# Optimization experiments

Hardware: AMD Instinct MI355X
Metric: run time of the kernel (lower is better)

## Reference

```python
import jax, jax.numpy as jnp
import numpy as np

B, S, H = 4, 1024, 1024
NH, HD = 16, 64  # num heads, head dim


def setup_inputs() -> dict:
    key = jax.random.key(0)
    ks = jax.random.split(key, 7)
    scale = 1.0 / np.sqrt(H)
    return {
        "hidden_states": jax.random.normal(ks[0], (B, S, H), jnp.float32),
        "attention_mask": jnp.zeros((B, 1, 1, S), jnp.float32),
        "Wq": jax.random.normal(ks[1], (H, H), jnp.float32) * scale,
        "bq": jnp.zeros((H,), jnp.float32),
        "Wk": jax.random.normal(ks[2], (H, H), jnp.float32) * scale,
        "bk": jnp.zeros((H,), jnp.float32),
        "Wv": jax.random.normal(ks[3], (H, H), jnp.float32) * scale,
        "bv": jnp.zeros((H,), jnp.float32),
    }


def _heads(x):
    # [B,S,H] -> [B,NH,S,HD]
    return x.reshape(x.shape[0], x.shape[1], NH, HD).transpose(0, 2, 1, 3)


def reference(hidden_states, attention_mask, Wq, bq, Wk, bk, Wv, bv):
    q = _heads(hidden_states @ Wq + bq)  # [B,NH,S,HD]
    k = _heads(hidden_states @ Wk + bk)
    v = _heads(hidden_states @ Wv + bv)
    scores = jnp.einsum("bhqd,bhkd->bhqk", q, k) / np.sqrt(HD)
    scores = scores + attention_mask  # broadcast additive mask
    probs = jax.nn.softmax(scores, axis=-1)  # dropout p=0 (eval)
    ctx = jnp.einsum("bhqk,bhkd->bhqd", probs, v)
    # [B,NH,S,HD] -> [B,S,H]
    return ctx.transpose(0, 2, 1, 3).reshape(hidden_states.shape[0], hidden_states.shape[1], NH * HD)
```

## Files before the change

### kernel.cpp

```cpp
#include <hip/hip_runtime.h>
#include <hip/hip_bf16.h>

typedef __bf16 bf16_t;
typedef __bf16 bf16x8 __attribute__((ext_vector_type(8)));
typedef float f32x4 __attribute__((ext_vector_type(4)));
typedef float f32x16 __attribute__((ext_vector_type(16)));
typedef unsigned uint2v __attribute__((ext_vector_type(2)));

#define MFMA16(a, b, c) __builtin_amdgcn_mfma_f32_16x16x32_bf16((a), (b), (c), 0, 0, 0)
#define MFMA32(a, b, c) __builtin_amdgcn_mfma_f32_32x32x16_bf16((a), (b), (c), 0, 0, 0)

static constexpr int BB = 4, SS = 1024, HH = 1024, NHEAD = 16, HDIM = 64;
static constexpr int MM = BB * SS;

__device__ __forceinline__ void gload_lds16(const void* g, void* l) {
  __builtin_amdgcn_global_load_lds((const __attribute__((address_space(1))) void*)g,
                                   (__attribute__((address_space(3))) void*)l, 16, 0, 0);
}

#if __has_builtin(__builtin_amdgcn_permlane32_swap)
#define PSWAP(a, b)                                                    \
  {                                                                    \
    uint2v _r = __builtin_amdgcn_permlane32_swap((a), (b), false, false); \
    (a) = _r.x;                                                        \
    (b) = _r.y;                                                        \
  }
#else
#define PSWAP(a, b) asm("v_permlane32_swap_b32 %0, %1" : "+v"(a), "+v"(b))
#endif

__global__ __launch_bounds__(256) void cvt_bf16_kernel(const float* __restrict__ in,
                                                       bf16_t* __restrict__ out, int n) {
  int i = (blockIdx.x * 256 + threadIdx.x) * 8;
  if (i >= n) return;
  float4 a = *(const float4*)(in + i);
  float4 b = *(const float4*)(in + i + 4);
  union { int4 i4; bf16_t h[8]; } u;
  u.h[0] = (bf16_t)a.x; u.h[1] = (bf16_t)a.y; u.h[2] = (bf16_t)a.z; u.h[3] = (bf16_t)a.w;
  u.h[4] = (bf16_t)b.x; u.h[5] = (bf16_t)b.y; u.h[6] = (bf16_t)b.z; u.h[7] = (bf16_t)b.w;
  *(int4*)(out + i) = u.i4;
}

__global__ __launch_bounds__(256) void transposeW_kernel(const float* __restrict__ Wq,
                                                         const float* __restrict__ Wk,
                                                         const float* __restrict__ Wv,
                                                         bf16_t* __restrict__ WT) {
  __shared__ float tile[32][33];
  int z = blockIdx.z;
  const float* W = (z == 0) ? Wq : (z == 1) ? Wk : Wv;
  bf16_t* Out = WT + (size_t)z * HH * HH;
  int tx = threadIdx.x, ty = threadIdx.y;
  int x0 = blockIdx.x * 32;
  int y0 = blockIdx.y * 32;
  for (int j = ty; j < 32; j += 8)
    tile[j][tx] = W[(size_t)(y0 + j) * HH + x0 + tx];
  __syncthreads();
  for (int j = ty; j < 32; j += 8)
    Out[(size_t)(x0 + j) * HH + y0 + tx] = (bf16_t)tile[tx][j];
}

#define BMT 128
#define BNT 384
#define BKT 64
#define NTL 16
#define BUFBYTES 65536

__global__ __launch_bounds__(512, 2) void qkv_gemm2(const bf16_t* __restrict__ hiddenB,
                                                    const bf16_t* __restrict__ WT,
                                                    const float* __restrict__ bq,
                                                    const float* __restrict__ bk,
                                                    const float* __restrict__ bv,
                                                    bf16_t* __restrict__ Qo,
                                                    bf16_t* __restrict__ Ko,
                                                    bf16_t* __restrict__ Vt) {
  __shared__ bf16_t smem[2 * BUFBYTES / 2];

  const int wg = blockIdx.x;
  const int id = (wg & 7) * 32 + (wg >> 3);
  const int nb = id & 7;
  const int mb = id >> 3;

  const int t = threadIdx.x;
  const int lane = t & 63;
  const int w = t >> 6;
  const int wr = w >> 2;
  const int wc = w & 3;
  const int lr = lane & 15;
  const int g4 = lane >> 4;

  const unsigned schunk = (((unsigned)(t & 7)) ^ ((unsigned)((t >> 3) & 7))) << 4;
  const char* Ag = (const char*)hiddenB + (size_t)(mb * BMT) * 2048;
  const char* Bg = (const char*)WT + (size_t)(nb * BNT) * 2048;

  auto stage = [&](const char* gb, int growbase, int kbyte, char* ldsdest) {
    gload_lds16(gb + (size_t)(growbase + (t >> 3)) * 2048 + kbyte + schunk,
                ldsdest + w * 1024);
  };
  const unsigned axor = ((unsigned)(lr & 7)) << 4;

  f32x4 acc[4][6] = {};

  {
    char* S0 = (char*)smem;
    stage(Ag, 0, 0, S0);
    stage(Ag, 64, 0, S0 + 8192);
#pragma unroll
    for (int i = 0; i < 6; ++i) stage(Bg, i * 64, 0, S0 + 16384 + i * 8192);
  }
  asm volatile("s_waitcnt vmcnt(0)" ::: "memory");
  __builtin_amdgcn_s_barrier();

  for (int j = 0; j < NTL; ++j) {
    const char* Ab = (const char*)smem + (j & 1) * BUFBYTES;
    const char* Bb = Ab + 16384;
    char* Sb = (char*)smem + ((j + 1) & 1) * BUFBYTES;
    const int kb = (j + 1) * 128;
    const bool st = (j + 1 < NTL);

    if (st) { stage(Ag, 0, kb, Sb); stage(Ag, 64, kb, Sb + 8192); }

    bf16x8 af[4][2];
#pragma unroll
    for (int mi = 0; mi < 4; ++mi)
#pragma unroll
      for (int ks = 0; ks < 2; ++ks)
        af[mi][ks] = *(const bf16x8*)(Ab + (size_t)(wr * 64 + mi * 16 + lr) * 128 +
                                      (((unsigned)(ks * 64 + g4 * 16)) ^ axor));

#pragma unroll
    for (int p = 0; p < 3; ++p) {
      if (st) {
        stage(Bg, (2 * p) * 64, kb, Sb + 16384 + (2 * p) * 8192);
        stage(Bg, (2 * p + 1) * 64, kb, Sb + 16384 + (2 * p + 1) * 8192);
      }
      bf16x8 b0[2], b1[2];
#pragma unroll
      for (int ks = 0; ks < 2; ++ks) {
        b0[ks] = *(const bf16x8*)(Bb + (size_t)(wc * 96 + (2 * p) * 16 + lr) * 128 +
                                  (((unsigned)(ks * 64 + g4 * 16)) ^ axor));
        b1[ks] = *(const bf16x8*)(Bb + (size_t)(wc * 96 + (2 * p + 1) * 16 + lr) * 128 +
                                  (((unsigned)(ks * 64 + g4 * 16)) ^ axor));
      }
      __builtin_amdgcn_s_setprio(1);
#pragma unroll
      for (int mi = 0; mi < 4; ++mi)
#pragma unroll
        for (int ks = 0; ks < 2; ++ks) {
          acc[mi][2 * p] = MFMA16(af[mi][ks], b0[ks], acc[mi][2 * p]);
          acc[mi][2 * p + 1] = MFMA16(af[mi][ks], b1[ks], acc[mi][2 * p + 1]);
        }
      __builtin_amdgcn_s_setprio(0);
    }

    if (st) {
      asm volatile("s_waitcnt vmcnt(0)" ::: "memory");
      __builtin_amdgcn_s_barrier();
    }
  }

#pragma unroll
  for (int ni = 0; ni < 6; ++ni) {
    int col = nb * BNT + wc * 96 + ni * 16 + lr;
    int z = col >> 10;
    int ci = col & 1023;
    const float* bias = (z == 0) ? bq : (z == 1) ? bk : bv;
    float bia = bias[ci];
    int hh = ci >> 6, d = ci & 63;
    if (z < 2) {
      bf16_t* Out = (z == 0) ? Qo : Ko;
#pragma unroll
      for (int mi = 0; mi < 4; ++mi) {
#pragma unroll
        for (int r = 0; r < 4; ++r) {
          int row = mb * BMT + wr * 64 + mi * 16 + g4 * 4 + r;
          int b = row >> 10, s = row & 1023;
          Out[((size_t)(b * NHEAD + hh) * SS + s) * HDIM + d] = (bf16_t)(acc[mi][ni][r] + bia);
        }
      }
    } else {
#pragma unroll
      for (int mi = 0; mi < 4; ++mi) {
        int row0 = mb * BMT + wr * 64 + mi * 16 + g4 * 4;
        int b = row0 >> 10, s0 = row0 & 1023;
        float v0 = acc[mi][ni][0] + bia, v1 = acc[mi][ni][1] + bia;
        float v2 = acc[mi][ni][2] + bia, v3 = acc[mi][ni][3] + bia;
        unsigned u0, u1;
        asm("v_cvt_pk_bf16_f32 %0, %1, %2" : "=v"(u0) : "v"(v0), "v"(v1));
        asm("v_cvt_pk_bf16_f32 %0, %1, %2" : "=v"(u1) : "v"(v2), "v"(v3));
        uint2 pv; pv.x = u0; pv.y = u1;
        *(uint2*)&Vt[((size_t)(b * NHEAD + hh) * HDIM + d) * SS + s0] = pv;
      }
    }
  }
}

__global__ __launch_bounds__(256) void attn4_kernel(const bf16_t* __restrict__ Q,
                                                    const bf16_t* __restrict__ K,
                                                    const bf16_t* __restrict__ Vt,
                                                    const float* __restrict__ mask,
                                                    float* __restrict__ out) {
  __shared__ bf16_t KVsm[3][2][64 * 64];
  __shared__ float Msm[SS];

  const int wg = blockIdx.x;
  const int id = (wg & 7) * 64 + (wg >> 3);
  const int xblk = id & 7;
  const int bh = id >> 3;

  const int b = bh >> 4;
  const int h = bh & 15;
  const int t = threadIdx.x;
  const int lane = t & 63;
  const int w = t >> 6;
  const int l31 = lane & 31;
  const int hi = lane >> 5;
  const int q0 = xblk * 128 + w * 32;

  const bf16_t* Qh = Q + (size_t)bh * SS * HDIM;
  const bf16_t* Kh = K + (size_t)bh * SS * HDIM;
  const bf16_t* Vh = Vt + (size_t)bh * HDIM * SS;

  *(float4*)&Msm[t * 4] = *(const float4*)&mask[(size_t)b * SS + t * 4];

  bf16x8 qb[4];
#pragma unroll
  for (int c = 0; c < 4; ++c) {
    bf16x8 q = *(const bf16x8*)&Qh[(size_t)(q0 + l31) * HDIM + c * 16 + hi * 8];
#pragma unroll
    for (int e = 0; e < 8; ++e) q[e] = (bf16_t)((float)q[e] * 0.125f);
    qb[c] = q;
  }

  const int srow = lane >> 3;
  const unsigned gcol = ((lane & 7) * 16) ^ (srow << 4);
  const unsigned swz = (unsigned)((l31 & 7) << 4);

  auto stageKV = [&](int tile, int buf) {
    const int kv0 = tile * 64;
#pragma unroll
    for (int i = 0; i < 2; ++i) {
      int rbase = w * 16 + i * 8;
      gload_lds16((const char*)Kh + (size_t)(kv0 + rbase + srow) * 128 + gcol,
                  (char*)&KVsm[buf][0][0] + (size_t)rbase * 128);
      gload_lds16((const char*)Vh + (size_t)(rbase + srow) * 2048 + (size_t)kv0 * 2 + gcol,
                  (char*)&KVsm[buf][1][0] + (size_t)rbase * 128);
    }
  };

  f32x16 acc0 = {}, acc1 = {};
  float m_run = -1e30f, l_run = 0.f;

  stageKV(0, 0);
  stageKV(1, 1);
  asm volatile("s_waitcnt vmcnt(4) lgkmcnt(0)" ::: "memory");
  __builtin_amdgcn_s_barrier();

  for (int tt = 0; tt < 16; ++tt) {
    if (tt + 2 < 16) stageKV(tt + 2, (tt + 2) % 3);
    const char* Kb = (const char*)&KVsm[tt % 3][0][0];
    const char* Vb = (const char*)&KVsm[tt % 3][1][0];
    const int kv0 = tt * 64;

#pragma unroll
    for (int j = 0; j < 2; ++j) {
      f32x16 st = {};
      __builtin_amdgcn_s_setprio(1);
#pragma unroll
      for (int c = 0; c < 4; ++c) {
        bf16x8 kf = *(const bf16x8*)(Kb + (size_t)(j * 32 + l31) * 128 +
                                     ((unsigned)(c * 32 + hi * 16) ^ swz));
        st = MFMA32(kf, qb[c], st);
      }
      __builtin_amdgcn_s_setprio(0);
#pragma unroll
      for (int k2 = 0; k2 < 8; ++k2) {
        int off = 8 * (k2 >> 1) + 4 * hi + 2 * (k2 & 1);
        float2 mk = *(const float2*)&Msm[kv0 + j * 32 + off];
        st[2 * k2] += mk.x;
        st[2 * k2 + 1] += mk.y;
      }
      float mj = st[0];
#pragma unroll
      for (int r = 1; r < 16; ++r) mj = fmaxf(mj, st[r]);
      mj = fmaxf(mj, __shfl_xor(mj, 32));
      if (!__all(mj <= m_run + 8.f)) {
        float mnew = fmaxf(m_run, mj);
        float corr = __expf(m_run - mnew);
#pragma unroll
        for (int r = 0; r < 16; ++r) { acc0[r] *= corr; acc1[r] *= corr; }
        l_run *= corr;
        m_run = mnew;
      }
      float ls = 0.f;
#pragma unroll
      for (int r = 0; r < 16; ++r) {
        float p = __expf(st[r] - m_run);
        st[r] = p;
        ls += p;
      }
      ls += __shfl_xor(ls, 32);
      l_run += ls;
      unsigned wd[8];
#pragma unroll
      for (int k2 = 0; k2 < 8; ++k2) {
        float lo = st[2 * k2], hip = st[2 * k2 + 1];
        unsigned r;
        asm("v_cvt_pk_bf16_f32 %0, %1, %2" : "=v"(r) : "v"(lo), "v"(hip));
        wd[k2] = r;
      }
      unsigned a0 = wd[0], b0 = wd[2]; PSWAP(a0, b0);
      unsigned a1 = wd[1], b1 = wd[3]; PSWAP(a1, b1);
      unsigned a2 = wd[4], b2 = wd[6]; PSWAP(a2, b2);
      unsigned a3 = wd[5], b3 = wd[7]; PSWAP(a3, b3);
      union { unsigned u[4]; bf16x8 v; } pf0, pf1;
      pf0.u[0] = a0; pf0.u[1] = a1; pf0.u[2] = b0; pf0.u[3] = b1;
      pf1.u[0] = a2; pf1.u[1] = a3; pf1.u[2] = b2; pf1.u[3] = b3;
      __builtin_amdgcn_s_setprio(1);
#pragma unroll
      for (int kvc = 0; kvc < 2; ++kvc) {
        bf16x8 pf = (kvc == 0) ? pf0.v : pf1.v;
#pragma unroll
        for (int dch = 0; dch < 2; ++dch) {
          bf16x8 vf = *(const bf16x8*)(Vb + (size_t)(dch * 32 + l31) * 128 +
                                       ((unsigned)(j * 64 + kvc * 32 + hi * 16) ^ swz));
          if (dch == 0) acc0 = MFMA32(vf, pf, acc0);
          else          acc1 = MFMA32(vf, pf, acc1);
        }
      }
      __builtin_amdgcn_s_setprio(0);
    }

    if (tt < 14) {
      asm volatile("s_waitcnt vmcnt(4)" ::: "memory");
      __builtin_amdgcn_s_barrier();
    } else if (tt == 14) {
      asm volatile("s_waitcnt vmcnt(0)" ::: "memory");
      __builtin_amdgcn_s_barrier();
    }
  }

  float rinv = 1.0f / l_run;
  int q = q0 + l31;
  float* ob = out + ((size_t)(b * SS + q)) * HH + h * HDIM;
#pragma unroll
  for (int g = 0; g < 4; ++g) {
    float4 o0, o1;
    o0.x = acc0[g * 4 + 0] * rinv; o0.y = acc0[g * 4 + 1] * rinv;
    o0.z = acc0[g * 4 + 2] * rinv; o0.w = acc0[g * 4 + 3] * rinv;
    o1.x = acc1[g * 4 + 0] * rinv; o1.y = acc1[g * 4 + 1] * rinv;
    o1.z = acc1[g * 4 + 2] * rinv; o1.w = acc1[g * 4 + 3] * rinv;
    *(float4*)&ob[g * 8 + 4 * hi] = o0;
    *(float4*)&ob[32 + g * 8 + 4 * hi] = o1;
  }
}

extern "C" void kernel_launch(void* const* d_in, const int* in_sizes, int n_in,
                              void* d_out, int out_size, void* d_ws, size_t ws_size,
                              hipStream_t stream) {
  const float* hs   = (const float*)d_in[0];
  const float* mask = (const float*)d_in[1];
  const float* Wq   = (const float*)d_in[2];
  const float* bq   = (const float*)d_in[3];
  const float* Wk   = (const float*)d_in[4];
  const float* bk   = (const float*)d_in[5];
  const float* Wv   = (const float*)d_in[6];
  const float* bv   = (const float*)d_in[7];
  float* out = (float*)d_out;

  char* ws = (char*)d_ws;
  bf16_t* hiddenB = (bf16_t*)ws;
  bf16_t* WT      = (bf16_t*)(ws + (size_t)8 * 1024 * 1024);
  bf16_t* Qb      = (bf16_t*)(ws + (size_t)14 * 1024 * 1024);
  bf16_t* Kb      = (bf16_t*)(ws + (size_t)22 * 1024 * 1024);
  bf16_t* Vt      = (bf16_t*)(ws + (size_t)30 * 1024 * 1024);

  cvt_bf16_kernel<<<MM * HH / (256 * 8), 256, 0, stream>>>(hs, hiddenB, MM * HH);
  transposeW_kernel<<<dim3(32, 32, 3), dim3(32, 8), 0, stream>>>(Wq, Wk, Wv, WT);
  qkv_gemm2<<<256, 512, 0, stream>>>(hiddenB, WT, bq, bk, bv, Qb, Kb, Vt);
  attn4_kernel<<<512, 256, 0, stream>>>(Qb, Kb, Vt, mask, out);
}
```

Before: 82.10 us.

## Use exp2 softmax with prescaled scores and process full 64-key tile per step

Folds log2(e) into the Q scaling and the mask so the softmax can call the native exp2 instruction instead of __expf. It also merges the two 32-key halves of each KV tile into one softmax step with a single max/rescale check and tree reductions, halving the online-softmax bookkeeping and exposing more independent MFMAs. This raises register pressure from two score accumulators live at once and changes rounding slightly, since log2(e) is folded into the bf16 Q values.

```diff
diff --git a/kernel.cpp b/kernel.cpp
--- a/kernel.cpp
+++ b/kernel.cpp
@@ -27,6 +27,16 @@
   }
 #else
 #define PSWAP(a, b) asm("v_permlane32_swap_b32 %0, %1" : "+v"(a), "+v"(b))
+#endif
+
+#if __has_builtin(__builtin_amdgcn_exp2f)
+__device__ __forceinline__ float EXP2(float x) { return __builtin_amdgcn_exp2f(x); }
+#else
+__device__ __forceinline__ float EXP2(float x) {
+  float r;
+  asm("v_exp_f32 %0, %1" : "=v"(r) : "v"(x));
+  return r;
+}
 #endif
 
 __global__ __launch_bounds__(256) void cvt_bf16_kernel(const float* __restrict__ in,
@@ -194,7 +204,7 @@
   }
 }
 
-__global__ __launch_bounds__(256) void attn4_kernel(const bf16_t* __restrict__ Q,
+__global__ __launch_bounds__(256) void attn5_kernel(const bf16_t* __restrict__ Q,
                                                     const bf16_t* __restrict__ K,
                                                     const bf16_t* __restrict__ Vt,
                                                     const float* __restrict__ mask,
@@ -220,14 +230,19 @@
   const bf16_t* Kh = K + (size_t)bh * SS * HDIM;
   const bf16_t* Vh = Vt + (size_t)bh * HDIM * SS;
 
-  *(float4*)&Msm[t * 4] = *(const float4*)&mask[(size_t)b * SS + t * 4];
+  const float L2E = 1.4426950408889634f;
+  {
+    float4 mv = *(const float4*)&mask[(size_t)b * SS + t * 4];
+    mv.x *= L2E; mv.y *= L2E; mv.z *= L2E; mv.w *= L2E;
+    *(float4*)&Msm[t * 4] = mv;
+  }
 
   bf16x8 qb[4];
 #pragma unroll
   for (int c = 0; c < 4; ++c) {
     bf16x8 q = *(const bf16x8*)&Qh[(size_t)(q0 + l31) * HDIM + c * 16 + hi * 8];
 #pragma unroll
-    for (int e = 0; e < 8; ++e) q[e] = (bf16_t)((float)q[e] * 0.125f);
+    for (int e = 0; e < 8; ++e) q[e] = (bf16_t)((float)q[e] * (0.125f * L2E));
     qb[c] = q;
   }
 
@@ -261,74 +276,116 @@
     const char* Vb = (const char*)&KVsm[tt % 3][1][0];
     const int kv0 = tt * 64;
 
-#pragma unroll
-    for (int j = 0; j < 2; ++j) {
-      f32x16 st = {};
-      __builtin_amdgcn_s_setprio(1);
-#pragma unroll
-      for (int c = 0; c < 4; ++c) {
-        bf16x8 kf = *(const bf16x8*)(Kb + (size_t)(j * 32 + l31) * 128 +
-                                     ((unsigned)(c * 32 + hi * 16) ^ swz));
-        st = MFMA32(kf, qb[c], st);
-      }
-      __builtin_amdgcn_s_setprio(0);
-#pragma unroll
-      for (int k2 = 0; k2 < 8; ++k2) {
-        int off = 8 * (k2 >> 1) + 4 * hi + 2 * (k2 & 1);
-        float2 mk = *(const float2*)&Msm[kv0 + j * 32 + off];
-        st[2 * k2] += mk.x;
-        st[2 * k2 + 1] += mk.y;
-      }
-      float mj = st[0];
-#pragma unroll
-      for (int r = 1; r < 16; ++r) mj = fmaxf(mj, st[r]);
-      mj = fmaxf(mj, __shfl_xor(mj, 32));
-      if (!__all(mj <= m_run + 8.f)) {
-        float mnew = fmaxf(m_run, mj);
-        float corr = __expf(m_run - mnew);
-#pragma unroll
-        for (int r = 0; r < 16; ++r) { acc0[r] *= corr; acc1[r] *= corr; }
-        l_run *= corr;
-        m_run = mnew;
-      }
-      float ls = 0.f;
-#pragma unroll
-      for (int r = 0; r < 16; ++r) {
-        float p = __expf(st[r] - m_run);
-        st[r] = p;
-        ls += p;
-      }
-      ls += __shfl_xor(ls, 32);
-      l_run += ls;
-      unsigned wd[8];
-#pragma unroll
-      for (int k2 = 0; k2 < 8; ++k2) {
-        float lo = st[2 * k2], hip = st[2 * k2 + 1];
-        unsigned r;
-        asm("v_cvt_pk_bf16_f32 %0, %1, %2" : "=v"(r) : "v"(lo), "v"(hip));
-        wd[k2] = r;
-      }
-      unsigned a0 = wd[0], b0 = wd[2]; PSWAP(a0, b0);
-      unsigned a1 = wd[1], b1 = wd[3]; PSWAP(a1, b1);
-      unsigned a2 = wd[4], b2 = wd[6]; PSWAP(a2, b2);
-      unsigned a3 = wd[5], b3 = wd[7]; PSWAP(a3, b3);
-      union { unsigned u[4]; bf16x8 v; } pf0, pf1;
-      pf0.u[0] = a0; pf0.u[1] = a1; pf0.u[2] = b0; pf0.u[3] = b1;
-      pf1.u[0] = a2; pf1.u[1] = a3; pf1.u[2] = b2; pf1.u[3] = b3;
-      __builtin_amdgcn_s_setprio(1);
-#pragma unroll
-      for (int kvc = 0; kvc < 2; ++kvc) {
-        bf16x8 pf = (kvc == 0) ? pf0.v : pf1.v;
-#pragma unroll
-        for (int dch = 0; dch < 2; ++dch) {
-          bf16x8 vf = *(const bf16x8*)(Vb + (size_t)(dch * 32 + l31) * 128 +
-                                       ((unsigned)(j * 64 + kvc * 32 + hi * 16) ^ swz));
-          if (dch == 0) acc0 = MFMA32(vf, pf, acc0);
-          else          acc1 = MFMA32(vf, pf, acc1);
-        }
-      }
-      __builtin_amdgcn_s_setprio(0);
-    }
+    f32x16 st0 = {}, st1 = {};
+    __builtin_amdgcn_s_setprio(1);
+#pragma unroll
+    for (int c = 0; c < 4; ++c) {
+      bf16x8 kf0 = *(const bf16x8*)(Kb + (size_t)l31 * 128 + ((unsigned)(c * 32 + hi * 16) ^ swz));
+      st0 = MFMA32(kf0, qb[c], st0);
+    }
+#pragma unroll
+    for (int c = 0; c < 4; ++c) {
+      bf16x8 kf1 = *(const bf16x8*)(Kb + (size_t)(32 + l31) * 128 + ((unsigned)(c * 32 + hi * 16) ^ swz));
+      st1 = MFMA32(kf1, qb[c], st1);
+    }
+    __builtin_amdgcn_s_setprio(0);
+
+#pragma unroll
+    for (int k2 = 0; k2 < 8; ++k2) {
+      int off = 8 * (k2 >> 1) + 4 * hi + 2 * (k2 & 1);
+      float2 m0v = *(const float2*)&Msm[kv0 + off];
+      float2 m1v = *(const float2*)&Msm[kv0 + 32 + off];
+      st0[2 * k2] += m0v.x; st0[2 * k2 + 1] += m0v.y;
+      st1[2 * k2] += m1v.x; st1[2 * k2 + 1] += m1v.y;
+    }
+
+    float v0 = fmaxf(st0[0], st1[0]),  v1 = fmaxf(st0[1], st1[1]);
+    float v2 = fmaxf(st0[2], st1[2]),  v3 = fmaxf(st0[3], st1[3]);
+    float v4 = fmaxf(st0[4], st1[4]),  v5 = fmaxf(st0[5], st1[5]);
+    float v6 = fmaxf(st0[6], st1[6]),  v7 = fmaxf(st0[7], st1[7]);
+    float v8 = fmaxf(st0[8], st1[8]),  v9 = fmaxf(st0[9], st1[9]);
+    float v10 = fmaxf(st0[10], st1[10]), v11 = fmaxf(st0[11], st1[11]);
+    float v12 = fmaxf(st0[12], st1[12]), v13 = fmaxf(st0[13], st1[13]);
+    float v14 = fmaxf(st0[14], st1[14]), v15 = fmaxf(st0[15], st1[15]);
+    float g0 = fmaxf(fmaxf(v0, v1), v2);
+    float g1 = fmaxf(fmaxf(v3, v4), v5);
+    float g2 = fmaxf(fmaxf(v6, v7), v8);
+    float g3 = fmaxf(fmaxf(v9, v10), v11);
+    float g4 = fmaxf(fmaxf(v12, v13), v14);
+    float mj = fmaxf(fmaxf(fmaxf(g0, g1), g2), fmaxf(fmaxf(g3, g4), v15));
+    mj = fmaxf(mj, __shfl_xor(mj, 32));
+
+    if (!__all(mj <= m_run + 8.f)) {
+      float mnew = fmaxf(m_run, mj);
+      float corr = EXP2(m_run - mnew);
+#pragma unroll
+      for (int r = 0; r < 16; ++r) { acc0[r] *= corr; acc1[r] *= corr; }
+      l_run *= corr;
+      m_run = mnew;
+    }
+
+#pragma unroll
+    for (int r = 0; r < 16; ++r) st0[r] = EXP2(st0[r] - m_run);
+#pragma unroll
+    for (int r = 0; r < 16; ++r) st1[r] = EXP2(st1[r] - m_run);
+
+    float s0 = (st0[0] + st1[0]) + (st0[1] + st1[1]);
+    float s1 = (st0[2] + st1[2]) + (st0[3] + st1[3]);
+    float s2 = (st0[4] + st1[4]) + (st0[5] + st1[5]);
+    float s3 = (st0[6] + st1[6]) + (st0[7] + st1[7]);
+    float s4 = (st0[8] + st1[8]) + (st0[9] + st1[9]);
+    float s5 = (st0[10] + st1[10]) + (st0[11] + st1[11]);
+    float s6 = (st0[12] + st1[12]) + (st0[13] + st1[13]);
+    float s7 = (st0[14] + st1[14]) + (st0[15] + st1[15]);
+    float ls = ((s0 + s1) + (s2 + s3)) + ((s4 + s5) + (s6 + s7));
+    ls += __shfl_xor(ls, 32);
+    l_run += ls;
+
+    unsigned wd0[8], wd1[8];
+#pragma unroll
+    for (int k2 = 0; k2 < 8; ++k2) {
+      unsigned r0, r1;
+      float a0f = st0[2 * k2], a1f = st0[2 * k2 + 1];
+      float b0f = st1[2 * k2], b1f = st1[2 * k2 + 1];
+      asm("v_cvt_pk_bf16_f32 %0, %1, %2" : "=v"(r0) : "v"(a0f), "v"(a1f));
+      asm("v_cvt_pk_bf16_f32 %0, %1, %2" : "=v"(r1) : "v"(b0f), "v"(b1f));
+      wd0[k2] = r0; wd1[k2] = r1;
+    }
+    unsigned a0 = wd0[0], b0 = wd0[2]; PSWAP(a0, b0);
+    unsigned a1 = wd0[1], b1 = wd0[3]; PSWAP(a1, b1);
+    unsigned a2 = wd0[4], b2 = wd0[6]; PSWAP(a2, b2);
+    unsigned a3 = wd0[5], b3 = wd0[7]; PSWAP(a3, b3);
+    unsigned c0 = wd1[0], d0 = wd1[2]; PSWAP(c0, d0);
+    unsigned c1 = wd1[1], d1 = wd1[3]; PSWAP(c1, d1);
+    unsigned c2 = wd1[4], d2 = wd1[6]; PSWAP(c2, d2);
+    unsigned c3 = wd1[5], d3 = wd1[7]; PSWAP(c3, d3);
+    union { unsigned u[4]; bf16x8 v; } pf0, pf1, pf2, pf3;
+    pf0.u[0] = a0; pf0.u[1] = a1; pf0.u[2] = b0; pf0.u[3] = b1;
+    pf1.u[0] = a2; pf1.u[1] = a3; pf1.u[2] = b2; pf1.u[3] = b3;
+    pf2.u[0] = c0; pf2.u[1] = c1; pf2.u[2] = d0; pf2.u[3] = d1;
+    pf3.u[0] = c2; pf3.u[1] = c3; pf3.u[2] = d2; pf3.u[3] = d3;
+
+    __builtin_amdgcn_s_setprio(1);
+    {
+      bf16x8 vf;
+      vf = *(const bf16x8*)(Vb + (size_t)(0 * 32 + l31) * 128 + ((unsigned)(0 * 64 + 0 * 32 + hi * 16) ^ swz));
+      acc0 = MFMA32(vf, pf0.v, acc0);
+      vf = *(const bf16x8*)(Vb + (size_t)(1 * 32 + l31) * 128 + ((unsigned)(0 * 64 + 0 * 32 + hi * 16) ^ swz));
+      acc1 = MFMA32(vf, pf0.v, acc1);
+      vf = *(const bf16x8*)(Vb + (size_t)(0 * 32 + l31) * 128 + ((unsigned)(0 * 64 + 1 * 32 + hi * 16) ^ swz));
+      acc0 = MFMA32(vf, pf1.v, acc0);
+      vf = *(const bf16x8*)(Vb + (size_t)(1 * 32 + l31) * 128 + ((unsigned)(0 * 64 + 1 * 32 + hi * 16) ^ swz));
+      acc1 = MFMA32(vf, pf1.v, acc1);
+      vf = *(const bf16x8*)(Vb + (size_t)(0 * 32 + l31) * 128 + ((unsigned)(1 * 64 + 0 * 32 + hi * 16) ^ swz));
+      acc0 = MFMA32(vf, pf2.v, acc0);
+      vf = *(const bf16x8*)(Vb + (size_t)(1 * 32 + l31) * 128 + ((unsigned)(1 * 64 + 0 * 32 + hi * 16) ^ swz));
+      acc1 = MFMA32(vf, pf2.v, acc1);
+      vf = *(const bf16x8*)(Vb + (size_t)(0 * 32 + l31) * 128 + ((unsigned)(1 * 64 + 1 * 32 + hi * 16) ^ swz));
+      acc0 = MFMA32(vf, pf3.v, acc0);
+      vf = *(const bf16x8*)(Vb + (size_t)(1 * 32 + l31) * 128 + ((unsigned)(1 * 64 + 1 * 32 + hi * 16) ^ swz));
+      acc1 = MFMA32(vf, pf3.v, acc1);
+    }
+    __builtin_amdgcn_s_setprio(0);
 
     if (tt < 14) {
       asm volatile("s_waitcnt vmcnt(4)" ::: "memory");
@@ -377,5 +434,5 @@
   cvt_bf16_kernel<<<MM * HH / (256 * 8), 256, 0, stream>>>(hs, hiddenB, MM * HH);
   transposeW_kernel<<<dim3(32, 32, 3), dim3(32, 8), 0, stream>>>(Wq, Wk, Wv, WT);
   qkv_gemm2<<<256, 512, 0, stream>>>(hiddenB, WT, bq, bk, bv, Qb, Kb, Vt);
-  attn4_kernel<<<512, 256, 0, stream>>>(Qb, Kb, Vt, mask, out);
-}
+  attn5_kernel<<<512, 256, 0, stream>>>(Qb, Kb, Vt, mask, out);
+}
```

Result: faster. 78.70 us (-4.1%).
